# Kernel tuning notes

Hardware: AMD Instinct MI355X
Metric: run time of the kernel (lower is better)

## Reference

```python
import jax, jax.numpy as jnp
import numpy as np

T, N, M, B = 512, 512, 256, 256

def setup_inputs() -> dict:
    key = jax.random.key(0)
    ks = jax.random.split(key, 6)
    h_t = jax.random.normal(ks[0], (1, B, M), dtype=jnp.float32)
    s_t = jax.random.normal(ks[1], (1, B, M), dtype=jnp.float32)
    data = jax.random.normal(ks[2], (B, T, N), dtype=jnp.float32)
    # torch Linear weight layout: (out_features, in_features)
    W_e = jax.random.normal(ks[3], (T, 2 * M), dtype=jnp.float32) / np.sqrt(2 * M)
    U_e = jax.random.normal(ks[4], (T, T), dtype=jnp.float32) / np.sqrt(T)
    v_e = jax.random.normal(ks[5], (1, T), dtype=jnp.float32) / np.sqrt(T)
    return {"h_t": h_t, "s_t": s_t, "data": data, "W_e": W_e, "U_e": U_e, "v_e": v_e}

def reference(h_t, s_t, data, W_e, U_e, v_e):
    # h_t, s_t: (1, B, m) -> (B, 2m); query is identical across the n repeats,
    # so project once and broadcast instead of materializing (B, n, 2m).
    query = jnp.concatenate([h_t[0], s_t[0]], axis=-1)          # (B, 2m)
    wq = query @ W_e.T                                          # (B, T)
    ud = jnp.einsum('btn,st->bns', data, U_e)                   # (B, n, T)
    alpha = jnp.tanh(wq[:, None, :] + ud)                       # (B, n, T)
    scores = jnp.einsum('bnt,t->bn', alpha, v_e[0])             # (B, n)
    attn = jax.nn.softmax(scores, axis=-1)[:, None, :]          # (B, 1, n)
    return attn
```

## Files before the change

### kernel.cpp

```cpp
#include <hip/hip_runtime.h>
#include <hip/hip_bf16.h>
#include <cmath>

#define T_DIM 512
#define N_DIM 512
#define M_DIM 256
#define B_DIM 256

typedef __bf16 bf16x8 __attribute__((ext_vector_type(8)));
typedef float  f32x4  __attribute__((ext_vector_type(4)));
typedef unsigned int u32;

__device__ __forceinline__ void gload16(const __bf16* g, __bf16* l) {
    __builtin_amdgcn_global_load_lds(
        (const __attribute__((address_space(1))) void*)g,
        (__attribute__((address_space(3))) void*)l, 16, 0, 0);
}

__global__ __launch_bounds__(256) void uconv_kernel(
    const float* __restrict__ U, __bf16* __restrict__ Uh)
{
    const int i = (blockIdx.x * 256 + threadIdx.x) * 2;
    float2 v = *(const float2*)(U + i);
    Uh[i]   = (__bf16)v.x;
    Uh[i+1] = (__bf16)v.y;
}

__global__ __launch_bounds__(256) void wq_kernel(
    const float* __restrict__ h_t, const float* __restrict__ s_t,
    const float* __restrict__ W_e, float* __restrict__ wq)
{
    __shared__ float q[2 * M_DIM];
    const int b = blockIdx.x;
    const int tid = threadIdx.x;
    q[tid]         = h_t[(size_t)b * M_DIM + tid];
    q[M_DIM + tid] = s_t[(size_t)b * M_DIM + tid];
    __syncthreads();
    for (int tt = tid; tt < T_DIM; tt += 256) {
        const float4* wrow = (const float4*)(W_e + (size_t)tt * (2 * M_DIM));
        float acc = 0.f;
        #pragma unroll 4
        for (int k4 = 0; k4 < (2 * M_DIM) / 4; ++k4) {
            float4 w = wrow[k4];
            acc += q[4*k4+0] * w.x + q[4*k4+1] * w.y
                 + q[4*k4+2] * w.z + q[4*k4+3] * w.w;
        }
        wq[(size_t)b * T_DIM + tt] = acc;
    }
}

__global__ __launch_bounds__(256, 2) void fused4_kernel(
    const float* __restrict__ data, const __bf16* __restrict__ Uh,
    const float* __restrict__ v_e, const float* __restrict__ wq,
    float* __restrict__ partial)
{
    __shared__ __align__(16) __bf16 As[2][128 * 32];
    __shared__ __align__(16) __bf16 Bs[2][256 * 32];
    __shared__ float sc[128];

    const int wg    = blockIdx.x;
    const int xcd   = wg & 7;
    const int local = wg >> 3;
    const int sh    = local & 1;
    const int p     = xcd + 8 * (local >> 1);
    const int b     = p >> 2;
    const int nb    = p & 3;

    const int tid  = threadIdx.x;
    const int lane = tid & 63;
    const int wid  = tid >> 6;
    const int wm   = wid >> 1;
    const int wn   = wid & 1;

    if (tid < 128) sc[tid] = 0.f;

    f32x4 acc[4][8];
    const f32x4 zero = {0.f, 0.f, 0.f, 0.f};
    #pragma unroll
    for (int i = 0; i < 4; ++i)
        #pragma unroll
        for (int j = 0; j < 8; ++j)
            acc[i][j] = zero;

    const float*  Ab = data + (size_t)b * T_DIM * N_DIM + nb * 128;
    const __bf16* Bb = Uh + (size_t)(sh * 256) * T_DIM;

    const int rp = tid >> 4;
    const int cg = tid & 15;
    const int n0 = cg * 8;
    const int swzk = (cg & 3) << 2;

    const int r0 = tid >> 2;
    const int ce = (tid & 3) * 8;

    const int fr = lane & 15;
    const int kb = (lane >> 4) * 8;

    int aoff[4];
    #pragma unroll
    for (int mi = 0; mi < 4; ++mi) {
        const int row = wm * 64 + mi * 16 + fr;
        aoff[mi] = (row * 32 + kb) ^ (((row >> 3) & 3) << 3);
    }
    int boff[8];
    #pragma unroll
    for (int ni = 0; ni < 8; ++ni)
        boff[ni] = (wn * 128 + ni * 16 + fr) * 32 + kb;

    const float* s0 = Ab + (size_t)(2 * rp) * N_DIM + n0;
    float4 pa0 = *(const float4*)s0;
    float4 pa1 = *(const float4*)(s0 + 4);
    float4 pa2 = *(const float4*)(s0 + N_DIM);
    float4 pa3 = *(const float4*)(s0 + N_DIM + 4);

    #pragma unroll
    for (int i = 0; i < 4; ++i)
        gload16(Bb + (size_t)(i * 64 + r0) * T_DIM + ce, &Bs[0][tid * 8] + i * 64 * 32);
    {
        u32* As32 = (u32*)As[0];
        const float lo_[8] = {pa0.x, pa0.y, pa0.z, pa0.w, pa1.x, pa1.y, pa1.z, pa1.w};
        const float hi_[8] = {pa2.x, pa2.y, pa2.z, pa2.w, pa3.x, pa3.y, pa3.z, pa3.w};
        #pragma unroll
        for (int j = 0; j < 8; ++j) {
            __bf16 l = (__bf16)lo_[j];
            __bf16 h = (__bf16)hi_[j];
            u32 w = ((u32)__builtin_bit_cast(unsigned short, h) << 16)
                  |  (u32)__builtin_bit_cast(unsigned short, l);
            As32[((n0 + j) * 16 + rp) ^ swzk] = w;
        }
    }
    {
        const float* sn = Ab + (size_t)(32 + 2 * rp) * N_DIM + n0;
        pa0 = *(const float4*)sn;
        pa1 = *(const float4*)(sn + 4);
        pa2 = *(const float4*)(sn + N_DIM);
        pa3 = *(const float4*)(sn + N_DIM + 4);
    }
    __syncthreads();

    int cur = 0;
    for (int k0 = 0; k0 < T_DIM; k0 += 32) {
        bf16x8 a[4], bv[8];
        #pragma unroll
        for (int mi = 0; mi < 4; ++mi)
            a[mi] = *(const bf16x8*)&As[cur][aoff[mi]];
        #pragma unroll
        for (int ni = 0; ni < 8; ++ni)
            bv[ni] = *(const bf16x8*)&Bs[cur][boff[ni]];

        if (k0 + 32 < T_DIM) {
            const int nxt = cur ^ 1;
            #pragma unroll
            for (int i = 0; i < 4; ++i)
                gload16(Bb + (size_t)(i * 64 + r0) * T_DIM + (k0 + 32) + ce,
                        &Bs[nxt][tid * 8] + i * 64 * 32);
            u32* As32 = (u32*)As[nxt];
            const float lo_[8] = {pa0.x, pa0.y, pa0.z, pa0.w, pa1.x, pa1.y, pa1.z, pa1.w};
            const float hi_[8] = {pa2.x, pa2.y, pa2.z, pa2.w, pa3.x, pa3.y, pa3.z, pa3.w};
            #pragma unroll
            for (int j = 0; j < 8; ++j) {
                __bf16 l = (__bf16)lo_[j];
                __bf16 h = (__bf16)hi_[j];
                u32 w = ((u32)__builtin_bit_cast(unsigned short, h) << 16)
                      |  (u32)__builtin_bit_cast(unsigned short, l);
                As32[((n0 + j) * 16 + rp) ^ swzk] = w;
            }
            if (k0 + 64 < T_DIM) {
                const float* sn = Ab + (size_t)(k0 + 64 + 2 * rp) * N_DIM + n0;
                pa0 = *(const float4*)sn;
                pa1 = *(const float4*)(sn + 4);
                pa2 = *(const float4*)(sn + N_DIM);
                pa3 = *(const float4*)(sn + N_DIM + 4);
            }
        }

        #pragma unroll
        for (int mi = 0; mi < 4; ++mi)
            #pragma unroll
            for (int ni = 0; ni < 8; ++ni)
                acc[mi][ni] = __builtin_amdgcn_mfma_f32_16x16x32_bf16(a[mi], bv[ni], acc[mi][ni], 0, 0, 0);

        __syncthreads();
        cur ^= 1;
    }

    float wqv[8], vev[8];
    #pragma unroll
    for (int ni = 0; ni < 8; ++ni) {
        const int scol = sh * 256 + wn * 128 + ni * 16 + fr;
        wqv[ni] = wq[(size_t)b * T_DIM + scol];
        vev[ni] = v_e[scol];
    }
    const int g = lane >> 4;
    #pragma unroll
    for (int mi = 0; mi < 4; ++mi) {
        #pragma unroll
        for (int rg = 0; rg < 4; ++rg) {
            float part = 0.f;
            #pragma unroll
            for (int ni = 0; ni < 8; ++ni)
                part += vev[ni] * tanhf(wqv[ni] + acc[mi][ni][rg]);
            part += __shfl_xor(part, 1);
            part += __shfl_xor(part, 2);
            part += __shfl_xor(part, 4);
            part += __shfl_xor(part, 8);
            if (fr == 0)
                atomicAdd(&sc[wm * 64 + mi * 16 + 4 * g + rg], part);
        }
    }
    __syncthreads();
    if (tid < 128)
        partial[((size_t)b * 2 + sh) * N_DIM + nb * 128 + tid] = sc[tid];
}

__global__ __launch_bounds__(512) void softmax_kernel(
    const float* __restrict__ partial, float* __restrict__ out)
{
    const int b = blockIdx.x;
    const int n = threadIdx.x;
    const float* p = partial + (size_t)b * 2 * N_DIM;
    float s = p[n] + p[N_DIM + n];

    float m = s;
    #pragma unroll
    for (int off = 1; off < 64; off <<= 1)
        m = fmaxf(m, __shfl_xor(m, off));
    __shared__ float red[8];
    const int wv = n >> 6;
    if ((n & 63) == 0) red[wv] = m;
    __syncthreads();
    float bm = red[0];
    #pragma unroll
    for (int i = 1; i < 8; ++i) bm = fmaxf(bm, red[i]);

    float e = expf(s - bm);
    float t = e;
    #pragma unroll
    for (int off = 1; off < 64; off <<= 1)
        t += __shfl_xor(t, off);
    __syncthreads();
    if ((n & 63) == 0) red[wv] = t;
    __syncthreads();
    float tot = 0.f;
    #pragma unroll
    for (int i = 0; i < 8; ++i) tot += red[i];

    out[(size_t)b * N_DIM + n] = e / tot;
}

extern "C" void kernel_launch(void* const* d_in, const int* in_sizes, int n_in,
                              void* d_out, int out_size, void* d_ws, size_t ws_size,
                              hipStream_t stream) {
    const float* h_t  = (const float*)d_in[0];
    const float* s_t  = (const float*)d_in[1];
    const float* data = (const float*)d_in[2];
    const float* W_e  = (const float*)d_in[3];
    const float* U_e  = (const float*)d_in[4];
    const float* v_e  = (const float*)d_in[5];
    float* out = (float*)d_out;

    const size_t wq_elems      = (size_t)B_DIM * T_DIM;
    const size_t partial_elems = (size_t)B_DIM * 2 * N_DIM;
    const size_t u_elems       = (size_t)T_DIM * T_DIM;

    float* wq      = (float*)d_ws;
    float* partial = wq + wq_elems;
    __bf16* Uh     = (__bf16*)(partial + partial_elems);

    wq_kernel<<<B_DIM, 256, 0, stream>>>(h_t, s_t, W_e, wq);
    uconv_kernel<<<(int)(u_elems / 512), 256, 0, stream>>>(U_e, Uh);
    fused4_kernel<<<B_DIM * 8, 256, 0, stream>>>(data, Uh, v_e, wq, partial);
    softmax_kernel<<<B_DIM, 512, 0, stream>>>(partial, out);
}
```

Baseline: 176.2 us.

## Peel last GEMM iteration, use partial vmcnt waits and setprio around MFMAs

The main k-loop's last iteration is peeled so the body no longer branches on prefetch. __syncthreads is replaced by explicit s_waitcnt vmcnt(4) plus a sched-barrier-fenced s_barrier, so the register prefetch of the next data rows can stay in flight across the barrier. MFMA blocks are wrapped in s_setprio(1) to favour matrix issue over other waves. The hand-written waitcnt counts assume a particular order of memory instructions, which is a correctness risk if the compiler reorders loads.

Result: slower. 188.6 us (+7.1%).

```diff
diff --git a/kernel.cpp b/kernel.cpp
--- a/kernel.cpp
+++ b/kernel.cpp
@@ -10,6 +10,12 @@
 typedef __bf16 bf16x8 __attribute__((ext_vector_type(8)));
 typedef float  f32x4  __attribute__((ext_vector_type(4)));
 typedef unsigned int u32;
+
+#define WAITVM4()  asm volatile("s_waitcnt vmcnt(4) lgkmcnt(0)" ::: "memory")
+#define WAITVM0()  asm volatile("s_waitcnt vmcnt(0) lgkmcnt(0)" ::: "memory")
+#define PHASE_BARRIER() do { __builtin_amdgcn_sched_barrier(0); \
+                             __builtin_amdgcn_s_barrier();      \
+                             __builtin_amdgcn_sched_barrier(0); } while (0)
 
 __device__ __forceinline__ void gload16(const __bf16* g, __bf16* l) {
     __builtin_amdgcn_global_load_lds(
@@ -49,7 +55,7 @@
     }
 }
 
-__global__ __launch_bounds__(256, 2) void fused4_kernel(
+__global__ __launch_bounds__(256, 2) void fused5_kernel(
     const float* __restrict__ data, const __bf16* __restrict__ Uh,
     const float* __restrict__ v_e, const float* __restrict__ wq,
     float* __restrict__ partial)
@@ -136,10 +142,13 @@
         pa2 = *(const float4*)(sn + N_DIM);
         pa3 = *(const float4*)(sn + N_DIM + 4);
     }
-    __syncthreads();
+    WAITVM4();
+    PHASE_BARRIER();
 
     int cur = 0;
-    for (int k0 = 0; k0 < T_DIM; k0 += 32) {
+    for (int k0 = 0; k0 < T_DIM - 32; k0 += 32) {
+        const int nxt = cur ^ 1;
+
         bf16x8 a[4], bv[8];
         #pragma unroll
         for (int mi = 0; mi < 4; ++mi)
@@ -148,12 +157,12 @@
         for (int ni = 0; ni < 8; ++ni)
             bv[ni] = *(const bf16x8*)&Bs[cur][boff[ni]];
 
-        if (k0 + 32 < T_DIM) {
-            const int nxt = cur ^ 1;
-            #pragma unroll
-            for (int i = 0; i < 4; ++i)
-                gload16(Bb + (size_t)(i * 64 + r0) * T_DIM + (k0 + 32) + ce,
-                        &Bs[nxt][tid * 8] + i * 64 * 32);
+        #pragma unroll
+        for (int i = 0; i < 4; ++i)
+            gload16(Bb + (size_t)(i * 64 + r0) * T_DIM + (k0 + 32) + ce,
+                    &Bs[nxt][tid * 8] + i * 64 * 32);
+
+        {
             u32* As32 = (u32*)As[nxt];
             const float lo_[8] = {pa0.x, pa0.y, pa0.z, pa0.w, pa1.x, pa1.y, pa1.z, pa1.w};
             const float hi_[8] = {pa2.x, pa2.y, pa2.z, pa2.w, pa3.x, pa3.y, pa3.z, pa3.w};
@@ -165,23 +174,45 @@
                       |  (u32)__builtin_bit_cast(unsigned short, l);
                 As32[((n0 + j) * 16 + rp) ^ swzk] = w;
             }
-            if (k0 + 64 < T_DIM) {
-                const float* sn = Ab + (size_t)(k0 + 64 + 2 * rp) * N_DIM + n0;
-                pa0 = *(const float4*)sn;
-                pa1 = *(const float4*)(sn + 4);
-                pa2 = *(const float4*)(sn + N_DIM);
-                pa3 = *(const float4*)(sn + N_DIM + 4);
-            }
-        }
-
+        }
+
+        const bool more = (k0 + 64 < T_DIM);
+        if (more) {
+            const float* sn = Ab + (size_t)(k0 + 64 + 2 * rp) * N_DIM + n0;
+            pa0 = *(const float4*)sn;
+            pa1 = *(const float4*)(sn + 4);
+            pa2 = *(const float4*)(sn + N_DIM);
+            pa3 = *(const float4*)(sn + N_DIM + 4);
+        }
+
+        __builtin_amdgcn_s_setprio(1);
         #pragma unroll
         for (int mi = 0; mi < 4; ++mi)
             #pragma unroll
             for (int ni = 0; ni < 8; ++ni)
                 acc[mi][ni] = __builtin_amdgcn_mfma_f32_16x16x32_bf16(a[mi], bv[ni], acc[mi][ni], 0, 0, 0);
-
-        __syncthreads();
-        cur ^= 1;
+        __builtin_amdgcn_s_setprio(0);
+
+        if (more) { WAITVM4(); } else { WAITVM0(); }
+        PHASE_BARRIER();
+        cur = nxt;
+    }
+
+    {
+        bf16x8 a[4], bv[8];
+        #pragma unroll
+        for (int mi = 0; mi < 4; ++mi)
+            a[mi] = *(const bf16x8*)&As[cur][aoff[mi]];
+        #pragma unroll
+        for (int ni = 0; ni < 8; ++ni)
+            bv[ni] = *(const bf16x8*)&Bs[cur][boff[ni]];
+        __builtin_amdgcn_s_setprio(1);
+        #pragma unroll
+        for (int mi = 0; mi < 4; ++mi)
+            #pragma unroll
+            for (int ni = 0; ni < 8; ++ni)
+                acc[mi][ni] = __builtin_amdgcn_mfma_f32_16x16x32_bf16(a[mi], bv[ni], acc[mi][ni], 0, 0, 0);
+        __builtin_amdgcn_s_setprio(0);
     }
 
     float wqv[8], vev[8];
@@ -269,6 +300,6 @@
 
     wq_kernel<<<B_DIM, 256, 0, stream>>>(h_t, s_t, W_e, wq);
     uconv_kernel<<<(int)(u_elems / 512), 256, 0, stream>>>(U_e, Uh);
-    fused4_kernel<<<B_DIM * 8, 256, 0, stream>>>(data, Uh, v_e, wq, partial);
+    fused5_kernel<<<B_DIM * 8, 256, 0, stream>>>(data, Uh, v_e, wq, partial);
     softmax_kernel<<<B_DIM, 512, 0, stream>>>(partial, out);
 }
```
